# Optimization experiments

Measured on AMD Instinct MI355X. Metric: run time of the kernel, lower is better.

## Reference

```python
import jax, jax.numpy as jnp
import numpy as np

L, D, H, K, M = 4, 512, 8, 10, 2048  # depth, dim, heads, relation bins, mlp_dim
DH = D // H
B, N = 4, 512
EPS = 1e-5


def setup_inputs() -> dict:
    key = jax.random.key(0)
    ks = jax.random.split(key, 12)
    s = lambda i, shape, scale: jax.random.normal(ks[i], shape, jnp.float32) * scale
    return {
        "x": s(0, (B, N, D), 1.0),
        "coord": jax.random.uniform(ks[1], (B, N, 2), dtype=jnp.float32) * 20.0,  # spread over ~K distance bins
        "ln1_g": jnp.ones((L, D)), "ln1_b": jnp.zeros((L, D)),
        "wq": s(2, (L, D, D), 0.02), "bq": jnp.zeros((L, D)),
        "wk": s(3, (L, D, D), 0.02), "bk": jnp.zeros((L, D)),
        "wv": s(4, (L, D, D), 0.02), "bv": jnp.zeros((L, D)),
        "wo": s(5, (L, D, D), 0.02), "bo": jnp.zeros((L, D)),
        "rel_k": s(6, (L, K, DH), 0.02), "rel_v": s(7, (L, K, DH), 0.02),
        "ln2_g": jnp.ones((L, D)), "ln2_b": jnp.zeros((L, D)),
        "w1": s(8, (L, D, M), 0.02), "b1": jnp.zeros((L, M)),
        "w2": s(9, (L, M, D), 0.02), "b2": jnp.zeros((L, D)),
        "lnf_g": jnp.ones((D,)), "lnf_b": jnp.zeros((D,)),
    }


def _ln(x, g, b):
    m = jnp.mean(x, -1, keepdims=True)
    v = jnp.mean((x - m) ** 2, -1, keepdims=True)
    return (x - m) * jax.lax.rsqrt(v + EPS) * g + b


def _forward(x, coord, ln1_g, ln1_b, wq, bq, wk, bk, wv, bv, wo, bo,
             rel_k, rel_v, ln2_g, ln2_b, w1, b1, w2, b2, lnf_g, lnf_b):
    b_, n_, _ = x.shape
    # pairwise Euclidean distances bucketized + clipped to K relation bins
    dist = jnp.linalg.norm(coord[:, :, None, :] - coord[:, None, :, :], axis=-1)  # [B,N,N]
    idx = jnp.clip(jnp.floor(dist), 0, K - 1).astype(jnp.int32)                   # [B,N,N]
    scale = DH ** -0.5
    for l in range(L):
        h = _ln(x, ln1_g[l], ln1_b[l])
        q = (h @ wq[l] + bq[l]).reshape(b_, n_, H, DH).transpose(0, 2, 1, 3)  # [B,H,N,DH]
        k = (h @ wk[l] + bk[l]).reshape(b_, n_, H, DH).transpose(0, 2, 1, 3)
        v = (h @ wv[l] + bv[l]).reshape(b_, n_, H, DH).transpose(0, 2, 1, 3)
        aK = rel_k[l][idx]  # [B,N,N,DH] relation key embeddings
        aV = rel_v[l][idx]  # [B,N,N,DH] relation value embeddings
        scores = (jnp.einsum('bhnd,bhmd->bhnm', q, k)
                  + jnp.einsum('bhnd,bnmd->bhnm', q, aK)) * scale
        attn = jax.nn.softmax(scores, axis=-1)  # [B,H,N,N]
        o = (jnp.einsum('bhnm,bhmd->bhnd', attn, v)
             + jnp.einsum('bhnm,bnmd->bhnd', attn, aV))
        o = o.transpose(0, 2, 1, 3).reshape(b_, n_, D) @ wo[l] + bo[l]
        x = o + x  # residual around attention
        h2 = _ln(x, ln2_g[l], ln2_b[l])
        x = jax.nn.gelu(h2 @ w1[l] + b1[l], approximate=False) @ w2[l] + b2[l] + x  # FFN residual
    return _ln(x, lnf_g, lnf_b)


def reference(x, coord, ln1_g, ln1_b, wq, bq, wk, bk, wv, bv, wo, bo,
              rel_k, rel_v, ln2_g, ln2_b, w1, b1, w2, b2, lnf_g, lnf_b):
    return _forward(x, coord, ln1_g, ln1_b, wq, bq, wk, bk, wv, bv, wo, bo,
                    rel_k, rel_v, ln2_g, ln2_b, w1, b1, w2, b2, lnf_g, lnf_b)
```

## Files before the change

### kernel.cpp

```cpp
#include <hip/hip_runtime.h>
#include <cmath>

constexpr int Bx = 4, Nx = 512, Dx = 512, Hx = 8, DHx = 64, Kx = 10, Mx = 2048, Lx = 4;
constexpr float EPSx = 1e-5f;
typedef unsigned short u16;
typedef __attribute__((ext_vector_type(8))) short short8;
typedef __attribute__((ext_vector_type(4))) float f32x4;

__device__ __forceinline__ u16 f2bf(float f) {
  unsigned u = __builtin_bit_cast(unsigned, f);
  return (u16)((u + 0x7fffu + ((u >> 16) & 1u)) >> 16);
}
__device__ __forceinline__ float bf2f(u16 h) {
  unsigned u = ((unsigned)h) << 16;
  return __builtin_bit_cast(float, u);
}
__device__ __forceinline__ void gload16(const void* g, void* l) {
  __builtin_amdgcn_global_load_lds((const __attribute__((address_space(1))) void*)g,
                                   (__attribute__((address_space(3))) void*)l, 16, 0, 0);
}
__device__ __forceinline__ float wave_max(float v) {
  #pragma unroll
  for (int off = 1; off < 64; off <<= 1) v = fmaxf(v, __shfl_xor(v, off));
  return v;
}
__device__ __forceinline__ float wave_sum(float v) {
  #pragma unroll
  for (int off = 1; off < 64; off <<= 1) v += __shfl_xor(v, off);
  return v;
}

__global__ __launch_bounds__(256) void idx_kernel(const float* __restrict__ coord,
                                                  unsigned char* __restrict__ idx8) {
  int t = blockIdx.x * 256 + threadIdx.x;
  int m = t % Nx;
  int n = (t / Nx) % Nx;
  int b = t / (Nx * Nx);
  float dx = coord[(b * Nx + n) * 2 + 0] - coord[(b * Nx + m) * 2 + 0];
  float dy = coord[(b * Nx + n) * 2 + 1] - coord[(b * Nx + m) * 2 + 1];
  float dist = sqrtf(dx * dx + dy * dy);
  int bin = (int)floorf(dist);
  bin = bin < 0 ? 0 : (bin > Kx - 1 ? Kx - 1 : bin);
  idx8[t] = (unsigned char)bin;
}

__global__ __launch_bounds__(256) void wsplitT_kernel(const float* __restrict__ W,
                                                      u16* __restrict__ Thi,
                                                      u16* __restrict__ Tlo,
                                                      int K, int N) {
  __shared__ float tile[32][33];
  int l = blockIdx.z;
  const float* Wl = W + (size_t)l * K * N;
  u16* hi = Thi + (size_t)l * K * N;
  u16* lo = Tlo + (size_t)l * K * N;
  int n0 = blockIdx.x * 32, k0 = blockIdx.y * 32;
  int tx = threadIdx.x & 31, ty = threadIdx.x >> 5;
  #pragma unroll
  for (int i = 0; i < 4; i++) {
    int kk = ty + i * 8;
    tile[kk][tx] = Wl[(size_t)(k0 + kk) * N + n0 + tx];
  }
  __syncthreads();
  #pragma unroll
  for (int i = 0; i < 4; i++) {
    int nn = ty + i * 8;
    float v = tile[tx][nn];
    u16 h = f2bf(v);
    hi[(size_t)(n0 + nn) * K + k0 + tx] = h;
    lo[(size_t)(n0 + nn) * K + k0 + tx] = f2bf(v - bf2f(h));
  }
}

__global__ __launch_bounds__(256) void ln_kernel(const float* __restrict__ x,
                                                 const float* __restrict__ g,
                                                 const float* __restrict__ bta,
                                                 float* __restrict__ out) {
  __shared__ float red[256];
  int row = blockIdx.x;
  int tid = threadIdx.x;
  const float2 v = reinterpret_cast<const float2*>(x + (size_t)row * Dx)[tid];

  red[tid] = v.x + v.y;
  __syncthreads();
  for (int s = 128; s > 0; s >>= 1) { if (tid < s) red[tid] += red[tid + s]; __syncthreads(); }
  float mean = red[0] * (1.0f / Dx);
  __syncthreads();

  float d0 = v.x - mean, d1 = v.y - mean;
  red[tid] = d0 * d0 + d1 * d1;
  __syncthreads();
  for (int s = 128; s > 0; s >>= 1) { if (tid < s) red[tid] += red[tid + s]; __syncthreads(); }
  float rstd = rsqrtf(red[0] * (1.0f / Dx) + EPSx);
  __syncthreads();

  float2 gg = reinterpret_cast<const float2*>(g)[tid];
  float2 bb = reinterpret_cast<const float2*>(bta)[tid];
  float2 o;
  o.x = d0 * rstd * gg.x + bb.x;
  o.y = d1 * rstd * gg.y + bb.y;
  reinterpret_cast<float2*>(out + (size_t)row * Dx)[tid] = o;
}

__global__ __launch_bounds__(256) void ln_split_kernel(const float* __restrict__ x,
                                                       const float* __restrict__ g,
                                                       const float* __restrict__ bta,
                                                       u16* __restrict__ hhi,
                                                       u16* __restrict__ hlo) {
  __shared__ float red[256];
  int row = blockIdx.x;
  int tid = threadIdx.x;
  const float2 v = reinterpret_cast<const float2*>(x + (size_t)row * Dx)[tid];

  red[tid] = v.x + v.y;
  __syncthreads();
  for (int s = 128; s > 0; s >>= 1) { if (tid < s) red[tid] += red[tid + s]; __syncthreads(); }
  float mean = red[0] * (1.0f / Dx);
  __syncthreads();

  float d0 = v.x - mean, d1 = v.y - mean;
  red[tid] = d0 * d0 + d1 * d1;
  __syncthreads();
  for (int s = 128; s > 0; s >>= 1) { if (tid < s) red[tid] += red[tid + s]; __syncthreads(); }
  float rstd = rsqrtf(red[0] * (1.0f / Dx) + EPSx);
  __syncthreads();

  float2 gg = reinterpret_cast<const float2*>(g)[tid];
  float2 bb = reinterpret_cast<const float2*>(bta)[tid];
  float ox = d0 * rstd * gg.x + bb.x;
  float oy = d1 * rstd * gg.y + bb.y;
  u16 hx = f2bf(ox), hy = f2bf(oy);
  ushort2 hv = {hx, hy};
  ushort2 lv = {f2bf(ox - bf2f(hx)), f2bf(oy - bf2f(hy))};
  reinterpret_cast<ushort2*>(hhi + (size_t)row * Dx)[tid] = hv;
  reinterpret_cast<ushort2*>(hlo + (size_t)row * Dx)[tid] = lv;
}

template <int BM, int BN, int EPI>
__global__ __launch_bounds__(256) void gemm_mfma(
    const u16* __restrict__ Ahi, const u16* __restrict__ Alo,
    const u16* __restrict__ Bhi, const u16* __restrict__ Blo,
    const float* __restrict__ bias,
    float* __restrict__ C, u16* __restrict__ Chi, u16* __restrict__ Clo,
    int M, int Nn, int Kk) {
  constexpr int FM = BM / 32, FN = BN / 32;
  __shared__ __align__(16) u16 lds[(BM + BN) * 64];
  u16* lAhi = lds;
  u16* lAlo = lds + BM * 32;
  u16* lBhi = lds + BM * 64;
  u16* lBlo = lds + BM * 64 + BN * 32;

  const int tid = threadIdx.x;
  const int lane = tid & 63;
  const int wid = tid >> 6;
  const int wr = wid >> 1, wc = wid & 1;
  const int row0 = blockIdx.y * BM, col0 = blockIdx.x * BN;
  const int kg = (lane >> 4) * 8;
  const int lr = lane & 15;

  f32x4 acc[FM][FN];
  #pragma unroll
  for (int m = 0; m < FM; m++)
    #pragma unroll
    for (int n = 0; n < FN; n++) acc[m][n] = (f32x4)(0.0f);

  constexpr int AR = (BM * 32) / 2048;
  constexpr int BR = (BN * 32) / 2048;

  for (int kt = 0; kt < Kk; kt += 32) {
    #pragma unroll
    for (int r = 0; r < AR; r++) {
      int e = r * 2048 + tid * 8;
      int row = e >> 5, kc = e & 31;
      size_t go = (size_t)(row0 + row) * Kk + kt + kc;
      gload16(Ahi + go, lAhi + e);
      gload16(Alo + go, lAlo + e);
    }
    #pragma unroll
    for (int r = 0; r < BR; r++) {
      int e = r * 2048 + tid * 8;
      int row = e >> 5, kc = e & 31;
      size_t go = (size_t)(col0 + row) * Kk + kt + kc;
      gload16(Bhi + go, lBhi + e);
      gload16(Blo + go, lBlo + e);
    }
    __syncthreads();

    short8 ah[FM], al[FM], bh[FN], bl[FN];
    #pragma unroll
    for (int m = 0; m < FM; m++) {
      int off = (wr * (BM / 2) + m * 16 + lr) * 32 + kg;
      ah[m] = *reinterpret_cast<const short8*>(lAhi + off);
      al[m] = *reinterpret_cast<const short8*>(lAlo + off);
    }
    #pragma unroll
    for (int n = 0; n < FN; n++) {
      int off = (wc * (BN / 2) + n * 16 + lr) * 32 + kg;
      bh[n] = *reinterpret_cast<const short8*>(lBhi + off);
      bl[n] = *reinterpret_cast<const short8*>(lBlo + off);
    }
    #pragma unroll
    for (int m = 0; m < FM; m++)
      #pragma unroll
      for (int n = 0; n < FN; n++) {
        acc[m][n] = __builtin_amdgcn_mfma_f32_16x16x32_bf16(ah[m], bh[n], acc[m][n], 0, 0, 0);
        acc[m][n] = __builtin_amdgcn_mfma_f32_16x16x32_bf16(ah[m], bl[n], acc[m][n], 0, 0, 0);
        acc[m][n] = __builtin_amdgcn_mfma_f32_16x16x32_bf16(al[m], bh[n], acc[m][n], 0, 0, 0);
      }
    __syncthreads();
  }

  const int rbase = (lane >> 4) * 4;
  #pragma unroll
  for (int m = 0; m < FM; m++) {
    #pragma unroll
    for (int n = 0; n < FN; n++) {
      int cidx = col0 + wc * (BN / 2) + n * 16 + lr;
      float bcol = bias[cidx];
      #pragma unroll
      for (int r = 0; r < 4; r++) {
        int row = row0 + wr * (BM / 2) + m * 16 + rbase + r;
        size_t o = (size_t)row * Nn + cidx;
        float val = acc[m][n][r] + bcol;
        if constexpr (EPI == 1) {
          C[o] = val + C[o];
        } else if constexpr (EPI == 2) {
          val = 0.5f * val * (1.0f + erff(val * 0.70710678118654752f));
          u16 h = f2bf(val);
          Chi[o] = h;
          Clo[o] = f2bf(val - bf2f(h));
        } else if constexpr (EPI == 3) {
          u16 h = f2bf(val);
          Chi[o] = h;
          Clo[o] = f2bf(val - bf2f(h));
        } else {
          size_t ot = (size_t)cidx * M + row;
          u16 h = f2bf(val);
          Chi[ot] = h;
          Clo[ot] = f2bf(val - bf2f(h));
        }
      }
    }
  }
}

__global__ __launch_bounds__(256) void qrel_kernel(const u16* __restrict__ qhi,
                                                   const u16* __restrict__ qlo,
                                                   const float* __restrict__ relk,
                                                   float* __restrict__ qrel) {
  int t = blockIdx.x * 256 + threadIdx.x;
  if (t >= Bx * Nx * Hx * Kx) return;
  int kbin = t % Kx;
  int h = (t / Kx) % Hx;
  int bn = t / (Kx * Hx);
  size_t base = (size_t)bn * Dx + h * DHx;
  const float* rr = relk + kbin * DHx;
  float s = 0.f;
  #pragma unroll
  for (int d = 0; d < DHx; d++)
    s += (bf2f(qhi[base + d]) + bf2f(qlo[base + d])) * rr[d];
  qrel[t] = s;
}

__global__ __launch_bounds__(256) void scores_mfma(
    const u16* __restrict__ qhi, const u16* __restrict__ qlo,
    const u16* __restrict__ khi, const u16* __restrict__ klo,
    const float* __restrict__ qrel, const unsigned char* __restrict__ idx8,
    float* __restrict__ scores) {
  __shared__ __align__(16) u16 lds[4 * 2048];
  u16* lQh = lds;
  u16* lQl = lds + 2048;
  u16* lKh = lds + 4096;
  u16* lKl = lds + 6144;

  const int bh = blockIdx.z;
  const int b = bh >> 3, h = bh & 7;
  const int n0 = blockIdx.y * 64, m0 = blockIdx.x * 64;
  const int tid = threadIdx.x;
  const int lane = tid & 63;
  const int wid = tid >> 6;
  const int wr = wid >> 1, wc = wid & 1;
  const int kg = (lane >> 4) * 8;
  const int lr = lane & 15;

  f32x4 acc[2][2];
  #pragma unroll
  for (int m = 0; m < 2; m++)
    #pragma unroll
    for (int n = 0; n < 2; n++) acc[m][n] = (f32x4)(0.0f);

  for (int kt = 0; kt < DHx; kt += 32) {
    int e = tid * 8;
    int row = e >> 5, kc = e & 31;
    size_t gq = (size_t)(b * Nx + n0 + row) * Dx + h * DHx + kt + kc;
    size_t gk = (size_t)(b * Nx + m0 + row) * Dx + h * DHx + kt + kc;
    gload16(qhi + gq, lQh + e);
    gload16(qlo + gq, lQl + e);
    gload16(khi + gk, lKh + e);
    gload16(klo + gk, lKl + e);
    __syncthreads();

    short8 ah[2], al[2], bhf[2], blf[2];
    #pragma unroll
    for (int m = 0; m < 2; m++) {
      int off = (wr * 32 + m * 16 + lr) * 32 + kg;
      ah[m] = *reinterpret_cast<const short8*>(lQh + off);
      al[m] = *reinterpret_cast<const short8*>(lQl + off);
    }
    #pragma unroll
    for (int n = 0; n < 2; n++) {
      int off = (wc * 32 + n * 16 + lr) * 32 + kg;
      bhf[n] = *reinterpret_cast<const short8*>(lKh + off);
      blf[n] = *reinterpret_cast<const short8*>(lKl + off);
    }
    #pragma unroll
    for (int m = 0; m < 2; m++)
      #pragma unroll
      for (int n = 0; n < 2; n++) {
        acc[m][n] = __builtin_amdgcn_mfma_f32_16x16x32_bf16(ah[m], bhf[n], acc[m][n], 0, 0, 0);
        acc[m][n] = __builtin_amdgcn_mfma_f32_16x16x32_bf16(ah[m], blf[n], acc[m][n], 0, 0, 0);
        acc[m][n] = __builtin_amdgcn_mfma_f32_16x16x32_bf16(al[m], bhf[n], acc[m][n], 0, 0, 0);
      }
    __syncthreads();
  }

  const int rbase = (lane >> 4) * 4;
  #pragma unroll
  for (int m = 0; m < 2; m++) {
    #pragma unroll
    for (int n = 0; n < 2; n++) {
      int mg = m0 + wc * 32 + n * 16 + lr;
      #pragma unroll
      for (int r = 0; r < 4; r++) {
        int ng = n0 + wr * 32 + m * 16 + rbase + r;
        unsigned char iv = idx8[(size_t)(b * Nx + ng) * Nx + mg];
        float bias = qrel[((size_t)(b * Nx + ng) * Hx + h) * Kx + iv];
        scores[((size_t)bh * Nx + ng) * Nx + mg] = (acc[m][n][r] + bias) * 0.125f;
      }
    }
  }
}

__global__ __launch_bounds__(256) void softmax_wave(float* scores,
                                                    const unsigned char* __restrict__ idx8,
                                                    float* __restrict__ attnK) {
  const int tid = threadIdx.x;
  const int lane = tid & 63;
  const int wid = tid >> 6;
  const int row = blockIdx.x * 4 + wid;
  const int n = row & (Nx - 1);
  const int b = row >> 12;
  float* s = scores + (size_t)row * Nx;

  float4 v0 = reinterpret_cast<const float4*>(s)[lane * 2];
  float4 v1 = reinterpret_cast<const float4*>(s)[lane * 2 + 1];
  float p[8] = {v0.x, v0.y, v0.z, v0.w, v1.x, v1.y, v1.z, v1.w};

  float mx = p[0];
  #pragma unroll
  for (int j = 1; j < 8; j++) mx = fmaxf(mx, p[j]);
  mx = wave_max(mx);

  float sum = 0.f;
  #pragma unroll
  for (int j = 0; j < 8; j++) { p[j] = expf(p[j] - mx); sum += p[j]; }
  sum = wave_sum(sum);
  float inv = 1.0f / sum;

  const unsigned char* idr = idx8 + (size_t)(b * Nx + n) * Nx + lane * 8;
  uchar4 c0 = *reinterpret_cast<const uchar4*>(idr);
  uchar4 c1 = *reinterpret_cast<const uchar4*>(idr + 4);
  int iv[8] = {c0.x, c0.y, c0.z, c0.w, c1.x, c1.y, c1.z, c1.w};

  float bins[Kx];
  #pragma unroll
  for (int kk = 0; kk < Kx; kk++) bins[kk] = 0.f;
  #pragma unroll
  for (int j = 0; j < 8; j++)
    #pragma unroll
    for (int kk = 0; kk < Kx; kk++) bins[kk] += (iv[j] == kk) ? p[j] : 0.f;
  #pragma unroll
  for (int kk = 0; kk < Kx; kk++) bins[kk] = wave_sum(bins[kk]);

  short8 sv;
  #pragma unroll
  for (int j = 0; j < 8; j++) sv[j] = (short)f2bf(p[j] * inv);
  u16* prow = reinterpret_cast<u16*>(s);
  *reinterpret_cast<short8*>(prow + lane * 8) = sv;

  if (lane == 0) {
    #pragma unroll
    for (int kk = 0; kk < Kx; kk++) attnK[(size_t)row * Kx + kk] = bins[kk] * inv;
  }
}

__global__ __launch_bounds__(256) void pv_mfma(
    const u16* __restrict__ P,
    const u16* __restrict__ vThi, const u16* __restrict__ vTlo,
    const float* __restrict__ attnK, const float* __restrict__ rel_v,
    u16* __restrict__ ohi, u16* __restrict__ olo) {
  __shared__ __align__(16) u16 lP[2048], lVh[2048], lVl[2048];
  __shared__ float aKs[64][Kx];
  __shared__ float RelVs[Kx][DHx];

  const int bh = blockIdx.y;
  const int b = bh >> 3, h = bh & 7;
  const int n0 = blockIdx.x * 64;
  const int tid = threadIdx.x;
  const int lane = tid & 63;
  const int wid = tid >> 6;
  const int wr = wid >> 1, wc = wid & 1;
  const int kg = (lane >> 4) * 8;
  const int lr = lane & 15;

  for (int t = tid; t < 64 * Kx; t += 256)
    aKs[t / Kx][t % Kx] = attnK[(size_t)(bh * Nx + n0 + t / Kx) * Kx + t % Kx];
  for (int t = tid; t < Kx * DHx; t += 256)
    RelVs[t / DHx][t % DHx] = rel_v[t];

  f32x4 acc[2][2];
  #pragma unroll
  for (int m = 0; m < 2; m++)
    #pragma unroll
    for (int n = 0; n < 2; n++) acc[m][n] = (f32x4)(0.0f);

  for (int mt = 0; mt < Nx; mt += 32) {
    int e = tid * 8;
    int row = e >> 5, kc = e & 31;
    gload16(P + (size_t)(bh * Nx + n0 + row) * 1024 + mt + kc, lP + e);
    size_t gv = (size_t)(h * DHx + row) * 2048 + b * Nx + mt + kc;
    gload16(vThi + gv, lVh + e);
    gload16(vTlo + gv, lVl + e);
    __syncthreads();

    short8 pa[2], bvh[2], bvl[2];
    #pragma unroll
    for (int m = 0; m < 2; m++) {
      int off = (wr * 32 + m * 16 + lr) * 32 + kg;
      pa[m] = *reinterpret_cast<const short8*>(lP + off);
    }
    #pragma unroll
    for (int n = 0; n < 2; n++) {
      int off = (wc * 32 + n * 16 + lr) * 32 + kg;
      bvh[n] = *reinterpret_cast<const short8*>(lVh + off);
      bvl[n] = *reinterpret_cast<const short8*>(lVl + off);
    }
    #pragma unroll
    for (int m = 0; m < 2; m++)
      #pragma unroll
      for (int n = 0; n < 2; n++) {
        acc[m][n] = __builtin_amdgcn_mfma_f32_16x16x32_bf16(pa[m], bvh[n], acc[m][n], 0, 0, 0);
        acc[m][n] = __builtin_amdgcn_mfma_f32_16x16x32_bf16(pa[m], bvl[n], acc[m][n], 0, 0, 0);
      }
    __syncthreads();
  }

  const int rbase = (lane >> 4) * 4;
  #pragma unroll
  for (int n = 0; n < 2; n++) {
    int dl = wc * 32 + n * 16 + lr;
    float rv[Kx];
    #pragma unroll
    for (int kk = 0; kk < Kx; kk++) rv[kk] = RelVs[kk][dl];
    #pragma unroll
    for (int m = 0; m < 2; m++) {
      #pragma unroll
      for (int r = 0; r < 4; r++) {
        int nl = wr * 32 + m * 16 + rbase + r;
        float val = acc[m][n][r];
        #pragma unroll
        for (int kk = 0; kk < Kx; kk++) val += aKs[nl][kk] * rv[kk];
        size_t oo = (size_t)(b * Nx + n0 + nl) * Dx + h * DHx + dl;
        u16 hh = f2bf(val);
        ohi[oo] = hh;
        olo[oo] = f2bf(val - bf2f(hh));
      }
    }
  }
}

extern "C" void kernel_launch(void* const* d_in, const int* in_sizes, int n_in,
                              void* d_out, int out_size, void* d_ws, size_t ws_size,
                              hipStream_t stream) {
  const float* x_in  = (const float*)d_in[0];
  const float* coord = (const float*)d_in[1];
  const float* ln1_g = (const float*)d_in[2];
  const float* ln1_b = (const float*)d_in[3];
  const float* wq    = (const float*)d_in[4];
  const float* bq    = (const float*)d_in[5];
  const float* wk    = (const float*)d_in[6];
  const float* bk    = (const float*)d_in[7];
  const float* wv    = (const float*)d_in[8];
  const float* bv    = (const float*)d_in[9];
  const float* wo    = (const float*)d_in[10];
  const float* bo    = (const float*)d_in[11];
  const float* rel_k = (const float*)d_in[12];
  const float* rel_v = (const float*)d_in[13];
  const float* ln2_g = (const float*)d_in[14];
  const float* ln2_b = (const float*)d_in[15];
  const float* w1    = (const float*)d_in[16];
  const float* b1    = (const float*)d_in[17];
  const float* w2    = (const float*)d_in[18];
  const float* b2    = (const float*)d_in[19];
  const float* lnf_g = (const float*)d_in[20];
  const float* lnf_b = (const float*)d_in[21];

  float* x = (float*)d_out;
  constexpr size_t BND  = (size_t)Bx * Nx * Dx;
  constexpr size_t SC   = (size_t)Bx * Hx * Nx * Nx;
  constexpr size_t RELS = (size_t)Bx * Nx * Hx * Kx;

  char* w = (char*)d_ws;
  size_t off = 0;
  auto nxt = [&](size_t bytes) -> void* {
    void* p = w + off;
    off = (off + bytes + 255) & ~(size_t)255;
    return p;
  };
  unsigned char* idxb = (unsigned char*)nxt((size_t)Bx * Nx * Nx);
  float* scores = (float*)nxt(4ull * SC);
  float* qrel   = (float*)nxt(4ull * RELS);
  float* attnK  = (float*)nxt(4ull * RELS);
  u16* qhi = (u16*)nxt(2ull * BND);
  u16* qlo = (u16*)nxt(2ull * BND);
  u16* khi = (u16*)nxt(2ull * BND);
  u16* klo = (u16*)nxt(2ull * BND);
  u16* vThi = (u16*)nxt(2ull * BND);
  u16* vTlo = (u16*)nxt(2ull * BND);
  u16* hhi = (u16*)nxt(2ull * BND);
  u16* hlo = (u16*)nxt(2ull * BND);
  u16* ohi = (u16*)nxt(2ull * BND);
  u16* olo = (u16*)nxt(2ull * BND);
  u16* wqThi = (u16*)nxt(2ull * Lx * Dx * Dx);
  u16* wqTlo = (u16*)nxt(2ull * Lx * Dx * Dx);
  u16* wkThi = (u16*)nxt(2ull * Lx * Dx * Dx);
  u16* wkTlo = (u16*)nxt(2ull * Lx * Dx * Dx);
  u16* wvThi = (u16*)nxt(2ull * Lx * Dx * Dx);
  u16* wvTlo = (u16*)nxt(2ull * Lx * Dx * Dx);
  u16* woThi = (u16*)nxt(2ull * Lx * Dx * Dx);
  u16* woTlo = (u16*)nxt(2ull * Lx * Dx * Dx);
  u16* w1Thi = (u16*)nxt(2ull * Lx * Dx * Mx);
  u16* w1Tlo = (u16*)nxt(2ull * Lx * Dx * Mx);
  u16* w2Thi = (u16*)nxt(2ull * Lx * Mx * Dx);
  u16* w2Tlo = (u16*)nxt(2ull * Lx * Mx * Dx);
  u16* f1hi = (u16*)scores;
  u16* f1lo = f1hi + (size_t)(Bx * Nx) * Mx;
  u16* Pbuf = (u16*)scores;

  hipMemcpyAsync(x, x_in, BND * sizeof(float), hipMemcpyDeviceToDevice, stream);
  idx_kernel<<<(Bx * Nx * Nx) / 256, 256, 0, stream>>>(coord, idxb);

  wsplitT_kernel<<<dim3(Dx / 32, Dx / 32, Lx), 256, 0, stream>>>(wq, wqThi, wqTlo, Dx, Dx);
  wsplitT_kernel<<<dim3(Dx / 32, Dx / 32, Lx), 256, 0, stream>>>(wk, wkThi, wkTlo, Dx, Dx);
  wsplitT_kernel<<<dim3(Dx / 32, Dx / 32, Lx), 256, 0, stream>>>(wv, wvThi, wvTlo, Dx, Dx);
  wsplitT_kernel<<<dim3(Dx / 32, Dx / 32, Lx), 256, 0, stream>>>(wo, woThi, woTlo, Dx, Dx);
  wsplitT_kernel<<<dim3(Mx / 32, Dx / 32, Lx), 256, 0, stream>>>(w1, w1Thi, w1Tlo, Dx, Mx);
  wsplitT_kernel<<<dim3(Dx / 32, Mx / 32, Lx), 256, 0, stream>>>(w2, w2Thi, w2Tlo, Mx, Dx);

  const int Mrows = Bx * Nx;
  dim3 g64(Dx / 64, Mrows / 64);
  dim3 g128(Mx / 128, Mrows / 128);
  dim3 gs(Nx / 64, Nx / 64, Bx * Hx);
  dim3 gpv(Nx / 64, Bx * Hx);

  for (int l = 0; l < Lx; l++) {
    size_t wD = (size_t)l * Dx * Dx;
    size_t w1o = (size_t)l * Dx * Mx;
    size_t w2o = (size_t)l * Mx * Dx;

    ln_split_kernel<<<Mrows, 256, 0, stream>>>(x, ln1_g + l * Dx, ln1_b + l * Dx, hhi, hlo);
    gemm_mfma<64, 64, 3><<<g64, 256, 0, stream>>>(hhi, hlo, wqThi + wD, wqTlo + wD,
                                                  bq + l * Dx, nullptr, qhi, qlo, Mrows, Dx, Dx);
    gemm_mfma<64, 64, 3><<<g64, 256, 0, stream>>>(hhi, hlo, wkThi + wD, wkTlo + wD,
                                                  bk + l * Dx, nullptr, khi, klo, Mrows, Dx, Dx);
    gemm_mfma<64, 64, 4><<<g64, 256, 0, stream>>>(hhi, hlo, wvThi + wD, wvTlo + wD,
                                                  bv + l * Dx, nullptr, vThi, vTlo, Mrows, Dx, Dx);
    qrel_kernel<<<(Bx * Nx * Hx * Kx + 255) / 256, 256, 0, stream>>>(
        qhi, qlo, rel_k + (size_t)l * Kx * DHx, qrel);
    scores_mfma<<<gs, 256, 0, stream>>>(qhi, qlo, khi, klo, qrel, idxb, scores);
    softmax_wave<<<Bx * Hx * Nx / 4, 256, 0, stream>>>(scores, idxb, attnK);
    pv_mfma<<<gpv, 256, 0, stream>>>(Pbuf, vThi, vTlo, attnK,
                                     rel_v + (size_t)l * Kx * DHx, ohi, olo);
    gemm_mfma<64, 64, 1><<<g64, 256, 0, stream>>>(ohi, olo, woThi + wD, woTlo + wD,
                                                  bo + l * Dx, x, nullptr, nullptr, Mrows, Dx, Dx);
    ln_split_kernel<<<Mrows, 256, 0, stream>>>(x, ln2_g + l * Dx, ln2_b + l * Dx, hhi, hlo);
    gemm_mfma<128, 128, 2><<<g128, 256, 0, stream>>>(hhi, hlo, w1Thi + w1o, w1Tlo + w1o,
                                                     b1 + l * Mx, nullptr, f1hi, f1lo, Mrows, Mx, Dx);
    gemm_mfma<64, 64, 1><<<g64, 256, 0, stream>>>(f1hi, f1lo, w2Thi + w2o, w2Tlo + w2o,
                                                  b2 + l * Dx, x, nullptr, nullptr, Mrows, Dx, Mx);
  }
  ln_kernel<<<Mrows, 256, 0, stream>>>(x, lnf_g, lnf_b, x);
}
```

Measured before the change: 946.9 us.

## Fuse QKV projections into one GEMM and split-K the residual GEMMs

Packs the transposed Q, K and V weights into one 1536-column matrix and computes all three projections in a single fused kernel, with the epilogue routing columns to q, k or transposed v. The Wo and W2 GEMMs now use a split-K kernel with 64x128 tiles and four K slices. Each slice atomically adds its partial sums into the residual, and only the first slice adds the bias. W1 switches to 64x128 tiles. The aim is fewer launches and more blocks in flight for the small-output GEMMs, at the cost of float atomics, which make the summation order nondeterministic.

```diff
diff --git a/kernel.cpp b/kernel.cpp
--- a/kernel.cpp
+++ b/kernel.cpp
@@ -47,12 +47,12 @@
 __global__ __launch_bounds__(256) void wsplitT_kernel(const float* __restrict__ W,
                                                       u16* __restrict__ Thi,
                                                       u16* __restrict__ Tlo,
-                                                      int K, int N) {
+                                                      int K, int N, size_t dst_lstride) {
   __shared__ float tile[32][33];
   int l = blockIdx.z;
   const float* Wl = W + (size_t)l * K * N;
-  u16* hi = Thi + (size_t)l * K * N;
-  u16* lo = Tlo + (size_t)l * K * N;
+  u16* hi = Thi + (size_t)l * dst_lstride;
+  u16* lo = Tlo + (size_t)l * dst_lstride;
   int n0 = blockIdx.x * 32, k0 = blockIdx.y * 32;
   int tx = threadIdx.x & 31, ty = threadIdx.x >> 5;
   #pragma unroll
@@ -228,15 +228,191 @@
           u16 h = f2bf(val);
           Chi[o] = h;
           Clo[o] = f2bf(val - bf2f(h));
-        } else if constexpr (EPI == 3) {
+        } else {
           u16 h = f2bf(val);
           Chi[o] = h;
           Clo[o] = f2bf(val - bf2f(h));
+        }
+      }
+    }
+  }
+}
+
+template <int KC>
+__global__ __launch_bounds__(256) void gemm_splitk(
+    const u16* __restrict__ Ahi, const u16* __restrict__ Alo,
+    const u16* __restrict__ Bhi, const u16* __restrict__ Blo,
+    const float* __restrict__ bias, float* __restrict__ C,
+    int M, int Nn, int Kk) {
+  constexpr int BM = 64, BN = 128;
+  constexpr int FM = 2, FN = 4;
+  __shared__ __align__(16) u16 lds[(BM + BN) * 64];
+  u16* lAhi = lds;
+  u16* lAlo = lds + BM * 32;
+  u16* lBhi = lds + BM * 64;
+  u16* lBlo = lds + BM * 64 + BN * 32;
+
+  const int tid = threadIdx.x;
+  const int lane = tid & 63;
+  const int wid = tid >> 6;
+  const int wr = wid >> 1, wc = wid & 1;
+  const int row0 = blockIdx.y * BM, col0 = blockIdx.x * BN;
+  const int kz = blockIdx.z;
+  const int kbase = kz * KC;
+  const int kg = (lane >> 4) * 8;
+  const int lr = lane & 15;
+
+  f32x4 acc[FM][FN];
+  #pragma unroll
+  for (int m = 0; m < FM; m++)
+    #pragma unroll
+    for (int n = 0; n < FN; n++) acc[m][n] = (f32x4)(0.0f);
+
+  for (int kt = kbase; kt < kbase + KC; kt += 32) {
+    {
+      int e = tid * 8;
+      int row = e >> 5, kc = e & 31;
+      size_t go = (size_t)(row0 + row) * Kk + kt + kc;
+      gload16(Ahi + go, lAhi + e);
+      gload16(Alo + go, lAlo + e);
+    }
+    #pragma unroll
+    for (int r = 0; r < 2; r++) {
+      int e = r * 2048 + tid * 8;
+      int row = e >> 5, kc = e & 31;
+      size_t go = (size_t)(col0 + row) * Kk + kt + kc;
+      gload16(Bhi + go, lBhi + e);
+      gload16(Blo + go, lBlo + e);
+    }
+    __syncthreads();
+
+    short8 ah[FM], al[FM], bh[FN], bl[FN];
+    #pragma unroll
+    for (int m = 0; m < FM; m++) {
+      int off = (wr * 32 + m * 16 + lr) * 32 + kg;
+      ah[m] = *reinterpret_cast<const short8*>(lAhi + off);
+      al[m] = *reinterpret_cast<const short8*>(lAlo + off);
+    }
+    #pragma unroll
+    for (int n = 0; n < FN; n++) {
+      int off = (wc * 64 + n * 16 + lr) * 32 + kg;
+      bh[n] = *reinterpret_cast<const short8*>(lBhi + off);
+      bl[n] = *reinterpret_cast<const short8*>(lBlo + off);
+    }
+    #pragma unroll
+    for (int m = 0; m < FM; m++)
+      #pragma unroll
+      for (int n = 0; n < FN; n++) {
+        acc[m][n] = __builtin_amdgcn_mfma_f32_16x16x32_bf16(ah[m], bh[n], acc[m][n], 0, 0, 0);
+        acc[m][n] = __builtin_amdgcn_mfma_f32_16x16x32_bf16(ah[m], bl[n], acc[m][n], 0, 0, 0);
+        acc[m][n] = __builtin_amdgcn_mfma_f32_16x16x32_bf16(al[m], bh[n], acc[m][n], 0, 0, 0);
+      }
+    __syncthreads();
+  }
+
+  const int rbase = (lane >> 4) * 4;
+  #pragma unroll
+  for (int m = 0; m < FM; m++) {
+    #pragma unroll
+    for (int n = 0; n < FN; n++) {
+      int cidx = col0 + wc * 64 + n * 16 + lr;
+      float bcol = (kz == 0) ? bias[cidx] : 0.0f;
+      #pragma unroll
+      for (int r = 0; r < 4; r++) {
+        int row = row0 + wr * 32 + m * 16 + rbase + r;
+        atomicAdd(&C[(size_t)row * Nn + cidx], acc[m][n][r] + bcol);
+      }
+    }
+  }
+}
+
+__global__ __launch_bounds__(256) void gemm_qkv(
+    const u16* __restrict__ Ahi, const u16* __restrict__ Alo,
+    const u16* __restrict__ Bhi, const u16* __restrict__ Blo,
+    const float* __restrict__ bq, const float* __restrict__ bk,
+    const float* __restrict__ bv,
+    u16* __restrict__ qhi, u16* __restrict__ qlo,
+    u16* __restrict__ khi, u16* __restrict__ klo,
+    u16* __restrict__ vThi, u16* __restrict__ vTlo) {
+  constexpr int Kk = 512;
+  __shared__ __align__(16) u16 lds[128 * 64];
+  u16* lAhi = lds;
+  u16* lAlo = lds + 2048;
+  u16* lBhi = lds + 4096;
+  u16* lBlo = lds + 6144;
+
+  const int tid = threadIdx.x;
+  const int lane = tid & 63;
+  const int wid = tid >> 6;
+  const int wr = wid >> 1, wc = wid & 1;
+  const int row0 = blockIdx.y * 64, col0 = blockIdx.x * 64;
+  const int kg = (lane >> 4) * 8;
+  const int lr = lane & 15;
+
+  f32x4 acc[2][2];
+  #pragma unroll
+  for (int m = 0; m < 2; m++)
+    #pragma unroll
+    for (int n = 0; n < 2; n++) acc[m][n] = (f32x4)(0.0f);
+
+  for (int kt = 0; kt < Kk; kt += 32) {
+    int e = tid * 8;
+    int row = e >> 5, kc = e & 31;
+    size_t ga = (size_t)(row0 + row) * Kk + kt + kc;
+    size_t gb = (size_t)(col0 + row) * Kk + kt + kc;
+    gload16(Ahi + ga, lAhi + e);
+    gload16(Alo + ga, lAlo + e);
+    gload16(Bhi + gb, lBhi + e);
+    gload16(Blo + gb, lBlo + e);
+    __syncthreads();
+
+    short8 ah[2], al[2], bh[2], bl[2];
+    #pragma unroll
+    for (int m = 0; m < 2; m++) {
+      int off = (wr * 32 + m * 16 + lr) * 32 + kg;
+      ah[m] = *reinterpret_cast<const short8*>(lAhi + off);
+      al[m] = *reinterpret_cast<const short8*>(lAlo + off);
+    }
+    #pragma unroll
+    for (int n = 0; n < 2; n++) {
+      int off = (wc * 32 + n * 16 + lr) * 32 + kg;
+      bh[n] = *reinterpret_cast<const short8*>(lBhi + off);
+      bl[n] = *reinterpret_cast<const short8*>(lBlo + off);
+    }
+    #pragma unroll
+    for (int m = 0; m < 2; m++)
+      #pragma unroll
+      for (int n = 0; n < 2; n++) {
+        acc[m][n] = __builtin_amdgcn_mfma_f32_16x16x32_bf16(ah[m], bh[n], acc[m][n], 0, 0, 0);
+        acc[m][n] = __builtin_amdgcn_mfma_f32_16x16x32_bf16(ah[m], bl[n], acc[m][n], 0, 0, 0);
+        acc[m][n] = __builtin_amdgcn_mfma_f32_16x16x32_bf16(al[m], bh[n], acc[m][n], 0, 0, 0);
+      }
+    __syncthreads();
+  }
+
+  const int rbase = (lane >> 4) * 4;
+  #pragma unroll
+  for (int m = 0; m < 2; m++) {
+    #pragma unroll
+    for (int n = 0; n < 2; n++) {
+      int cidx = col0 + wc * 32 + n * 16 + lr;
+      float bcol = cidx < 512 ? bq[cidx]
+                  : (cidx < 1024 ? bk[cidx - 512] : bv[cidx - 1024]);
+      #pragma unroll
+      for (int r = 0; r < 4; r++) {
+        int row = row0 + wr * 32 + m * 16 + rbase + r;
+        float val = acc[m][n][r] + bcol;
+        u16 h = f2bf(val);
+        u16 lo2 = f2bf(val - bf2f(h));
+        if (cidx < 512) {
+          size_t o = (size_t)row * 512 + cidx;
+          qhi[o] = h; qlo[o] = lo2;
+        } else if (cidx < 1024) {
+          size_t o = (size_t)row * 512 + (cidx - 512);
+          khi[o] = h; klo[o] = lo2;
         } else {
-          size_t ot = (size_t)cidx * M + row;
-          u16 h = f2bf(val);
-          Chi[ot] = h;
-          Clo[ot] = f2bf(val - bf2f(h));
+          size_t o = (size_t)(cidx - 1024) * 2048 + row;
+          vThi[o] = h; vTlo[o] = lo2;
         }
       }
     }
@@ -508,6 +684,7 @@
   constexpr size_t BND  = (size_t)Bx * Nx * Dx;
   constexpr size_t SC   = (size_t)Bx * Hx * Nx * Nx;
   constexpr size_t RELS = (size_t)Bx * Nx * Hx * Kx;
+  constexpr size_t QKVW = (size_t)1536 * 512;
 
   char* w = (char*)d_ws;
   size_t off = 0;
@@ -530,12 +707,8 @@
   u16* hlo = (u16*)nxt(2ull * BND);
   u16* ohi = (u16*)nxt(2ull * BND);
   u16* olo = (u16*)nxt(2ull * BND);
-  u16* wqThi = (u16*)nxt(2ull * Lx * Dx * Dx);
-  u16* wqTlo = (u16*)nxt(2ull * Lx * Dx * Dx);
-  u16* wkThi = (u16*)nxt(2ull * Lx * Dx * Dx);
-  u16* wkTlo = (u16*)nxt(2ull * Lx * Dx * Dx);
-  u16* wvThi = (u16*)nxt(2ull * Lx * Dx * Dx);
-  u16* wvTlo = (u16*)nxt(2ull * Lx * Dx * Dx);
+  u16* wqkvThi = (u16*)nxt(2ull * Lx * QKVW);
+  u16* wqkvTlo = (u16*)nxt(2ull * Lx * QKVW);
   u16* woThi = (u16*)nxt(2ull * Lx * Dx * Dx);
   u16* woTlo = (u16*)nxt(2ull * Lx * Dx * Dx);
   u16* w1Thi = (u16*)nxt(2ull * Lx * Dx * Mx);
@@ -549,16 +722,23 @@
   hipMemcpyAsync(x, x_in, BND * sizeof(float), hipMemcpyDeviceToDevice, stream);
   idx_kernel<<<(Bx * Nx * Nx) / 256, 256, 0, stream>>>(coord, idxb);
 
-  wsplitT_kernel<<<dim3(Dx / 32, Dx / 32, Lx), 256, 0, stream>>>(wq, wqThi, wqTlo, Dx, Dx);
-  wsplitT_kernel<<<dim3(Dx / 32, Dx / 32, Lx), 256, 0, stream>>>(wk, wkThi, wkTlo, Dx, Dx);
-  wsplitT_kernel<<<dim3(Dx / 32, Dx / 32, Lx), 256, 0, stream>>>(wv, wvThi, wvTlo, Dx, Dx);
-  wsplitT_kernel<<<dim3(Dx / 32, Dx / 32, Lx), 256, 0, stream>>>(wo, woThi, woTlo, Dx, Dx);
-  wsplitT_kernel<<<dim3(Mx / 32, Dx / 32, Lx), 256, 0, stream>>>(w1, w1Thi, w1Tlo, Dx, Mx);
-  wsplitT_kernel<<<dim3(Dx / 32, Mx / 32, Lx), 256, 0, stream>>>(w2, w2Thi, w2Tlo, Mx, Dx);
+  dim3 gw(Dx / 32, Dx / 32, Lx);
+  wsplitT_kernel<<<gw, 256, 0, stream>>>(wq, wqkvThi, wqkvTlo, Dx, Dx, QKVW);
+  wsplitT_kernel<<<gw, 256, 0, stream>>>(wk, wqkvThi + (size_t)512 * 512,
+                                         wqkvTlo + (size_t)512 * 512, Dx, Dx, QKVW);
+  wsplitT_kernel<<<gw, 256, 0, stream>>>(wv, wqkvThi + (size_t)1024 * 512,
+                                         wqkvTlo + (size_t)1024 * 512, Dx, Dx, QKVW);
+  wsplitT_kernel<<<gw, 256, 0, stream>>>(wo, woThi, woTlo, Dx, Dx, (size_t)Dx * Dx);
+  wsplitT_kernel<<<dim3(Mx / 32, Dx / 32, Lx), 256, 0, stream>>>(
+      w1, w1Thi, w1Tlo, Dx, Mx, (size_t)Dx * Mx);
+  wsplitT_kernel<<<dim3(Dx / 32, Mx / 32, Lx), 256, 0, stream>>>(
+      w2, w2Thi, w2Tlo, Mx, Dx, (size_t)Mx * Dx);
 
   const int Mrows = Bx * Nx;
-  dim3 g64(Dx / 64, Mrows / 64);
-  dim3 g128(Mx / 128, Mrows / 128);
+  dim3 gqkv(1536 / 64, Mrows / 64);
+  dim3 gw1(Mx / 128, Mrows / 64);
+  dim3 gwo(Dx / 128, Mrows / 64, 4);
+  dim3 gw2(Dx / 128, Mrows / 64, 4);
   dim3 gs(Nx / 64, Nx / 64, Bx * Hx);
   dim3 gpv(Nx / 64, Bx * Hx);
 
@@ -568,25 +748,24 @@
     size_t w2o = (size_t)l * Mx * Dx;
 
     ln_split_kernel<<<Mrows, 256, 0, stream>>>(x, ln1_g + l * Dx, ln1_b + l * Dx, hhi, hlo);
-    gemm_mfma<64, 64, 3><<<g64, 256, 0, stream>>>(hhi, hlo, wqThi + wD, wqTlo + wD,
-                                                  bq + l * Dx, nullptr, qhi, qlo, Mrows, Dx, Dx);
-    gemm_mfma<64, 64, 3><<<g64, 256, 0, stream>>>(hhi, hlo, wkThi + wD, wkTlo + wD,
-                                                  bk + l * Dx, nullptr, khi, klo, Mrows, Dx, Dx);
-    gemm_mfma<64, 64, 4><<<g64, 256, 0, stream>>>(hhi, hlo, wvThi + wD, wvTlo + wD,
-                                                  bv + l * Dx, nullptr, vThi, vTlo, Mrows, Dx, Dx);
+    gemm_qkv<<<gqkv, 256, 0, stream>>>(hhi, hlo,
+                                       wqkvThi + (size_t)l * QKVW, wqkvTlo + (size_t)l * QKVW,
+                                       bq + l * Dx, bk + l * Dx, bv + l * Dx,
+                                       qhi, qlo, khi, klo, vThi, vTlo);
     qrel_kernel<<<(Bx * Nx * Hx * Kx + 255) / 256, 256, 0, stream>>>(
         qhi, qlo, rel_k + (size_t)l * Kx * DHx, qrel);
     scores_mfma<<<gs, 256, 0, stream>>>(qhi, qlo, khi, klo, qrel, idxb, scores);
     softmax_wave<<<Bx * Hx * Nx / 4, 256, 0, stream>>>(scores, idxb, attnK);
     pv_mfma<<<gpv, 256, 0, stream>>>(Pbuf, vThi, vTlo, attnK,
                                      rel_v + (size_t)l * Kx * DHx, ohi, olo);
-    gemm_mfma<64, 64, 1><<<g64, 256, 0, stream>>>(ohi, olo, woThi + wD, woTlo + wD,
-                                                  bo + l * Dx, x, nullptr, nullptr, Mrows, Dx, Dx);
+    gemm_splitk<128><<<gwo, 256, 0, stream>>>(ohi, olo, woThi + wD, woTlo + wD,
+                                              bo + l * Dx, x, Mrows, Dx, Dx);
     ln_split_kernel<<<Mrows, 256, 0, stream>>>(x, ln2_g + l * Dx, ln2_b + l * Dx, hhi, hlo);
-    gemm_mfma<128, 128, 2><<<g128, 256, 0, stream>>>(hhi, hlo, w1Thi + w1o, w1Tlo + w1o,
-                                                     b1 + l * Mx, nullptr, f1hi, f1lo, Mrows, Mx, Dx);
-    gemm_mfma<64, 64, 1><<<g64, 256, 0, stream>>>(f1hi, f1lo, w2Thi + w2o, w2Tlo + w2o,
-                                                  b2 + l * Dx, x, nullptr, nullptr, Mrows, Dx, Mx);
+    gemm_mfma<64, 128, 2><<<gw1, 256, 0, stream>>>(hhi, hlo, w1Thi + w1o, w1Tlo + w1o,
+                                                   b1 + l * Mx, nullptr, f1hi, f1lo,
+                                                   Mrows, Mx, Dx);
+    gemm_splitk<512><<<gw2, 256, 0, stream>>>(f1hi, f1lo, w2Thi + w2o, w2Tlo + w2o,
+                                              b2 + l * Dx, x, Mrows, Dx, Mx);
   }
   ln_kernel<<<Mrows, 256, 0, stream>>>(x, lnf_g, lnf_b, x);
 }
```

After: 793.7 us. 1.19x faster.
